# Kernel tuning notes

Hardware: AMD Instinct MI355X
Metric: run time of the kernel (lower is better)

## Reference

```python
import jax, jax.numpy as jnp
import numpy as np

B, T, H, OUT = 65536, 24, 64, 2  # batch, window, num_neurons, 2*predicted_step
P_LAYER, P_TIME = 0.2, 0.2


def _mask(k, p):
    # bernoulli(1-p)/(1-p) variational dropout mask on [B, H]
    return jax.random.bernoulli(k, 1.0 - p, (B, H)).astype(jnp.float32) / (1.0 - p)


def setup_inputs() -> dict:
    key = jax.random.key(0)
    ks = jax.random.split(key, 20)
    u = 1.0 / np.sqrt(H)  # torch LSTMCell default init: U(-1/sqrt(H), 1/sqrt(H))
    xav = np.sqrt(2.0 / (B + H))  # xavier_normal_ std for [B, H] states
    inp = {
        "x": jax.random.normal(ks[0], (B, T, 1), dtype=jnp.float32),
        # LSTMCell 1: input dim 1 -> H; gates stacked [i, f, g, o] like torch
        "W_ih1": jax.random.uniform(ks[1], (4 * H, 1), minval=-u, maxval=u),
        "W_hh1": jax.random.uniform(ks[2], (4 * H, H), minval=-u, maxval=u),
        "b_ih1": jax.random.uniform(ks[3], (4 * H,), minval=-u, maxval=u),
        "b_hh1": jax.random.uniform(ks[4], (4 * H,), minval=-u, maxval=u),
        # LSTMCell 2: H -> H
        "W_ih2": jax.random.uniform(ks[5], (4 * H, H), minval=-u, maxval=u),
        "W_hh2": jax.random.uniform(ks[6], (4 * H, H), minval=-u, maxval=u),
        "b_ih2": jax.random.uniform(ks[7], (4 * H,), minval=-u, maxval=u),
        "b_hh2": jax.random.uniform(ks[8], (4 * H,), minval=-u, maxval=u),
        # output Linear H -> 2, bias hard-set to [0.2, -0.2]
        "W_out": jax.random.uniform(ks[9], (OUT, H), minval=-u, maxval=u),
        "b_out": jnp.array([0.2, -0.2], dtype=jnp.float32),
        # xavier_normal_ initialized states
        "h1_0": jax.random.normal(ks[10], (B, H)) * xav,
        "c1_0": jax.random.normal(ks[11], (B, H)) * xav,
        "h2_0": jax.random.normal(ks[12], (B, H)) * xav,
        "c2_0": jax.random.normal(ks[13], (B, H)) * xav,
        # variational dropout masks, fixed across timesteps
        "m_time1": _mask(ks[14], P_TIME),
        "m_time2": _mask(ks[15], P_TIME),
        "m_layer1": _mask(ks[16], P_LAYER),
        "m_layer2": _mask(ks[17], P_LAYER),
    }
    return inp


def _lstm_cell(x, h, c, W_ih, W_hh, b_ih, b_hh):
    gates = x @ W_ih.T + b_ih + h @ W_hh.T + b_hh  # [B, 4H]
    i, f, g, o = jnp.split(gates, 4, axis=-1)
    c_new = jax.nn.sigmoid(f) * c + jax.nn.sigmoid(i) * jnp.tanh(g)
    h_new = jax.nn.sigmoid(o) * jnp.tanh(c_new)
    return h_new, c_new


def reference(x, W_ih1, W_hh1, b_ih1, b_hh1, W_ih2, W_hh2, b_ih2, b_hh2,
              W_out, b_out, h1_0, c1_0, h2_0, c2_0,
              m_time1, m_time2, m_layer1, m_layer2):
    xs = jnp.transpose(x, (1, 0, 2))  # [T, B, 1]

    def step(carry, x_t):
        h1, c1, h2, c2 = carry
        h1, c1 = _lstm_cell(x_t, h1 * m_time1, c1, W_ih1, W_hh1, b_ih1, b_hh1)
        h1 = h1 * m_layer1
        h2, c2 = _lstm_cell(h1, h2 * m_time2, c2, W_ih2, W_hh2, b_ih2, b_hh2)
        h2 = h2 * m_layer2
        return (h1, c1, h2, c2), None

    (h1, c1, h2, c2), _ = jax.lax.scan(step, (h1_0, c1_0, h2_0, c2_0), xs)
    return h2 @ W_out.T + b_out  # [B, 2]
```

## Files before the change

kernel.cpp:

```cpp
#include <hip/hip_runtime.h>


typedef short short8v __attribute__((ext_vector_type(8)));
typedef float f32x4 __attribute__((ext_vector_type(4)));

#define LOG2E 1.44269504088896340736f

__device__ inline float gsig(float y){
  return __builtin_amdgcn_rcpf(1.0f + __builtin_amdgcn_exp2f(y));
}
__device__ inline float gtanh(float y){
  float s = __builtin_amdgcn_rcpf(1.0f + __builtin_amdgcn_exp2f(y));
  return fmaf(-2.0f, s, 1.0f);
}
__device__ inline float ftanh(float x){
  float e = __builtin_amdgcn_exp2f((2.0f * LOG2E) * x);
  return fmaf(-2.0f, __builtin_amdgcn_rcpf(1.0f + e), 1.0f);
}
__device__ inline unsigned short bf16c(float f){
  unsigned uu = __builtin_bit_cast(unsigned, f);
  uu = (uu + 0x7fffu + ((uu >> 16) & 1u)) >> 16;
  return (unsigned short)uu;
}

#define PK_STORE4(T, I, f0, f1, f2, f3) do{                       \
    unsigned _w01, _w23;                                          \
    asm("v_cvt_pk_bf16_f32 %0, %1, %2" : "=v"(_w01) : "v"(f0), "v"(f1)); \
    asm("v_cvt_pk_bf16_f32 %0, %1, %2" : "=v"(_w23) : "v"(f2), "v"(f3)); \
    (T)[(I)[0]] = (unsigned short)_w01;                           \
    (T)[(I)[1]] = (unsigned short)(_w01 >> 16);                   \
    (T)[(I)[2]] = (unsigned short)_w23;                           \
    (T)[(I)[3]] = (unsigned short)(_w23 >> 16);                   \
  }while(0)

__global__ __launch_bounds__(256, 2) void vlstm_kernel(
    const float* __restrict__ x,
    const float* __restrict__ Wih1, const float* __restrict__ Whh1,
    const float* __restrict__ bih1, const float* __restrict__ bhh1,
    const float* __restrict__ Wih2, const float* __restrict__ Whh2,
    const float* __restrict__ bih2, const float* __restrict__ bhh2,
    const float* __restrict__ Wout, const float* __restrict__ bout,
    const float* __restrict__ h10, const float* __restrict__ c10,
    const float* __restrict__ h20, const float* __restrict__ c20,
    const float* __restrict__ mt1v, const float* __restrict__ mt2v,
    const float* __restrict__ ml1v, const float* __restrict__ ml2v,
    float* __restrict__ out)
{
  __shared__ unsigned short sh1L[2][1024];
  __shared__ unsigned short sh1T[2][1024];
  __shared__ unsigned short sh2T[2][1024];
  __shared__ float h2f[1024];
  __shared__ float xlds[384];

  const int tid = threadIdx.x;
  const int w  = tid >> 6;
  const int l  = tid & 63;
  const int hi = l >> 4;
  const int lo = l & 15;
  const int u  = 16 * w + lo;

  float b1v[4], b2v[4], wiv[4];
  short8v fr1[4][2], frI[4][2], frH[4][2];
#pragma unroll
  for (int j = 0; j < 4; ++j){
    const float sc = (j == 2) ? (2.0f * LOG2E) : (-LOG2E);
    int n = u + 64 * j;
    b1v[j] = sc * (bih1[n] + bhh1[n]);
    b2v[j] = sc * (bih2[n] + bhh2[n]);
    wiv[j] = sc * Wih1[n];
#pragma unroll
    for (int kk = 0; kk < 2; ++kk){
      int off = n * 64 + 32 * kk + 8 * hi;
      short8v s;
#pragma unroll
      for (int e = 0; e < 8; ++e) s[e] = (short)bf16c(sc * Whh1[off + e]);
      fr1[j][kk] = s;
#pragma unroll
      for (int e = 0; e < 8; ++e) s[e] = (short)bf16c(sc * Wih2[off + e]);
      frI[j][kk] = s;
#pragma unroll
      for (int e = 0; e < 8; ++e) s[e] = (short)bf16c(sc * Whh2[off + e]);
      frH[j][kk] = s;
    }
  }

  int wIdx[4];
#pragma unroll
  for (int r = 0; r < 4; ++r){
    int m = 4 * hi + r;
    wIdx[r] = ((m * 128 + u * 2) ^ ((m & 7) << 4)) >> 1;
  }
  int rIdx[2];
#pragma unroll
  for (int kk = 0; kk < 2; ++kk){
    rIdx[kk] = ((lo * 128 + kk * 64 + hi * 16) ^ ((lo & 7) << 4)) >> 1;
  }

  const int row0 = blockIdx.x * 16;

  for (int idx = tid; idx < 384; idx += 256){
    int r = idx / 24, tt = idx - r * 24;
    xlds[tt * 16 + r] = x[(row0 + r) * 24 + tt];
  }
  float c1r[4], c2r[4], ml1r[4], ml2r[4], mt1r[4], mt2r[4];
  float h1i[4], h2i[4];
#pragma unroll
  for (int r = 0; r < 4; ++r){
    int gofs = (row0 + 4 * hi + r) * 64 + u;
    c1r[r]  = c10[gofs];  c2r[r]  = c20[gofs];
    ml1r[r] = ml1v[gofs]; ml2r[r] = ml2v[gofs];
    mt1r[r] = mt1v[gofs]; mt2r[r] = mt2v[gofs];
    h1i[r] = h10[gofs] * mt1r[r];
    h2i[r] = h20[gofs] * mt2r[r];
  }
  PK_STORE4(sh1T[0], wIdx, h1i[0], h1i[1], h1i[2], h1i[3]);
  PK_STORE4(sh2T[0], wIdx, h2i[0], h2i[1], h2i[2], h2i[3]);
  __syncthreads();

  short8v a1[2], at2[2];
  a1[0] = *(const short8v*)&sh1T[0][rIdx[0]];
  a1[1] = *(const short8v*)&sh1T[0][rIdx[1]];

  int P = 0;
#pragma unroll 1
  for (int t = 0; t < 24; ++t){
    const int Q = P ^ 1;
    f32x4 xv = *(const f32x4*)&xlds[t * 16 + 4 * hi];

    f32x4 gt[4];
#pragma unroll
    for (int j = 0; j < 4; ++j){
      f32x4 acc;
#pragma unroll
      for (int r = 0; r < 4; ++r) acc[r] = fmaf(xv[r], wiv[j], b1v[j]);
      acc = __builtin_amdgcn_mfma_f32_16x16x32_bf16(a1[0], fr1[j][0], acc, 0, 0, 0);
      acc = __builtin_amdgcn_mfma_f32_16x16x32_bf16(a1[1], fr1[j][1], acc, 0, 0, 0);
      gt[j] = acc;
    }
    float h1l[4], h1t[4];
#pragma unroll
    for (int r = 0; r < 4; ++r){
      float ti = gsig(gt[0][r]);
      float tf = gsig(gt[1][r]);
      float tg = gtanh(gt[2][r]);
      float to = gsig(gt[3][r]);
      float cn = fmaf(tf, c1r[r], ti * tg);
      c1r[r] = cn;
      h1l[r] = to * ftanh(cn) * ml1r[r];
      h1t[r] = h1l[r] * mt1r[r];
    }
    PK_STORE4(sh1L[Q], wIdx, h1l[0], h1l[1], h1l[2], h1l[3]);
    PK_STORE4(sh1T[Q], wIdx, h1t[0], h1t[1], h1t[2], h1t[3]);

    __syncthreads();

    short8v a2[2];
    a2[0]  = *(const short8v*)&sh1L[Q][rIdx[0]];
    a2[1]  = *(const short8v*)&sh1L[Q][rIdx[1]];
    a1[0]  = *(const short8v*)&sh1T[Q][rIdx[0]];
    a1[1]  = *(const short8v*)&sh1T[Q][rIdx[1]];
    at2[0] = *(const short8v*)&sh2T[P][rIdx[0]];
    at2[1] = *(const short8v*)&sh2T[P][rIdx[1]];

#pragma unroll
    for (int j = 0; j < 4; ++j){
      f32x4 acc;
#pragma unroll
      for (int r = 0; r < 4; ++r) acc[r] = b2v[j];
      acc = __builtin_amdgcn_mfma_f32_16x16x32_bf16(a2[0],  frI[j][0], acc, 0, 0, 0);
      acc = __builtin_amdgcn_mfma_f32_16x16x32_bf16(a2[1],  frI[j][1], acc, 0, 0, 0);
      acc = __builtin_amdgcn_mfma_f32_16x16x32_bf16(at2[0], frH[j][0], acc, 0, 0, 0);
      acc = __builtin_amdgcn_mfma_f32_16x16x32_bf16(at2[1], frH[j][1], acc, 0, 0, 0);
      gt[j] = acc;
    }
    float h2t[4];
#pragma unroll
    for (int r = 0; r < 4; ++r){
      float ti = gsig(gt[0][r]);
      float tf = gsig(gt[1][r]);
      float tg = gtanh(gt[2][r]);
      float to = gsig(gt[3][r]);
      float cn = fmaf(tf, c2r[r], ti * tg);
      c2r[r] = cn;
      float h2l = to * ftanh(cn) * ml2r[r];
      h2t[r] = h2l * mt2r[r];
      if (t == 23) h2f[(4 * hi + r) * 64 + u] = h2l;
    }
    PK_STORE4(sh2T[Q], wIdx, h2t[0], h2t[1], h2t[2], h2t[3]);

    P = Q;
  }
  __syncthreads();

  if (tid < 32){
    int r = tid & 15, o = tid >> 4;
    float acc = bout[o];
#pragma unroll 8
    for (int uu = 0; uu < 64; ++uu)
      acc = fmaf(h2f[r * 64 + uu], Wout[o * 64 + uu], acc);
    out[(row0 + r) * 2 + o] = acc;
  }
}

extern "C" void kernel_launch(void* const* d_in, const int* in_sizes, int n_in,
                              void* d_out, int out_size, void* d_ws, size_t ws_size,
                              hipStream_t stream)
{
  vlstm_kernel<<<dim3(4096), dim3(256), 0, stream>>>(
      (const float*)d_in[0],  (const float*)d_in[1],  (const float*)d_in[2],
      (const float*)d_in[3],  (const float*)d_in[4],  (const float*)d_in[5],
      (const float*)d_in[6],  (const float*)d_in[7],  (const float*)d_in[8],
      (const float*)d_in[9],  (const float*)d_in[10], (const float*)d_in[11],
      (const float*)d_in[12], (const float*)d_in[13], (const float*)d_in[14],
      (const float*)d_in[15], (const float*)d_in[16], (const float*)d_in[17],
      (const float*)d_in[18], (float*)d_out);
}
```

Before: 351.4 us.

## Raise occupancy to three blocks per CU via AGPR weights and packed masks

Raises the launch-bounds minimum from two to three blocks per CU. To fit the register budget it forces most bf16 weight fragments into AGPRs through an empty asm constraint and packs the four dropout masks into bf16 pairs, unpacked on each use. The aim is more resident waves to hide MFMA and transcendental latency in the serial recurrence. Each step now pays extra unpack ALU work, AGPR-to-VGPR moves may appear, and bf16 masks stay exact only because the mask values (0 and 1.25) are representable.

```diff
diff --git a/kernel.cpp b/kernel.cpp
--- a/kernel.cpp
+++ b/kernel.cpp
@@ -21,6 +21,10 @@
   unsigned uu = __builtin_bit_cast(unsigned, f);
   uu = (uu + 0x7fffu + ((uu >> 16) & 1u)) >> 16;
   return (unsigned short)uu;
+}
+__device__ inline float unpk(unsigned p, int h){
+  unsigned b = h ? (p & 0xffff0000u) : (p << 16);
+  return __builtin_bit_cast(float, b);
 }
 
 #define PK_STORE4(T, I, f0, f1, f2, f3) do{                       \
@@ -33,7 +37,7 @@
     (T)[(I)[3]] = (unsigned short)(_w23 >> 16);                   \
   }while(0)
 
-__global__ __launch_bounds__(256, 2) void vlstm_kernel(
+__global__ __launch_bounds__(256, 3) void vlstm_kernel(
     const float* __restrict__ x,
     const float* __restrict__ Wih1, const float* __restrict__ Whh1,
     const float* __restrict__ bih1, const float* __restrict__ bhh1,
@@ -84,6 +88,14 @@
     }
   }
 
+  asm volatile("" :
+    "+a"(fr1[0][0]), "+a"(fr1[0][1]), "+a"(fr1[1][0]), "+a"(fr1[1][1]),
+    "+a"(fr1[2][0]), "+a"(fr1[2][1]), "+a"(fr1[3][0]), "+a"(fr1[3][1]),
+    "+a"(frI[0][0]), "+a"(frI[0][1]), "+a"(frI[1][0]), "+a"(frI[1][1]),
+    "+a"(frI[2][0]), "+a"(frI[2][1]), "+a"(frI[3][0]), "+a"(frI[3][1]),
+    "+a"(frH[0][0]), "+a"(frH[0][1]), "+a"(frH[1][0]), "+a"(frH[1][1]),
+    "+a"(frH[2][0]));
+
   int wIdx[4];
 #pragma unroll
   for (int r = 0; r < 4; ++r){
@@ -102,19 +114,29 @@
     int r = idx / 24, tt = idx - r * 24;
     xlds[tt * 16 + r] = x[(row0 + r) * 24 + tt];
   }
-  float c1r[4], c2r[4], ml1r[4], ml2r[4], mt1r[4], mt2r[4];
-  float h1i[4], h2i[4];
-#pragma unroll
-  for (int r = 0; r < 4; ++r){
-    int gofs = (row0 + 4 * hi + r) * 64 + u;
-    c1r[r]  = c10[gofs];  c2r[r]  = c20[gofs];
-    ml1r[r] = ml1v[gofs]; ml2r[r] = ml2v[gofs];
-    mt1r[r] = mt1v[gofs]; mt2r[r] = mt2v[gofs];
-    h1i[r] = h10[gofs] * mt1r[r];
-    h2i[r] = h20[gofs] * mt2r[r];
-  }
-  PK_STORE4(sh1T[0], wIdx, h1i[0], h1i[1], h1i[2], h1i[3]);
-  PK_STORE4(sh2T[0], wIdx, h2i[0], h2i[1], h2i[2], h2i[3]);
+  float c1r[4], c2r[4];
+  unsigned ml1p[2], mt1p[2], ml2p[2], mt2p[2];
+  {
+    float mlt1[4], mtt1[4], mlt2[4], mtt2[4], h1i[4], h2i[4];
+#pragma unroll
+    for (int r = 0; r < 4; ++r){
+      int gofs = (row0 + 4 * hi + r) * 64 + u;
+      c1r[r]  = c10[gofs];  c2r[r]  = c20[gofs];
+      mlt1[r] = ml1v[gofs]; mlt2[r] = ml2v[gofs];
+      mtt1[r] = mt1v[gofs]; mtt2[r] = mt2v[gofs];
+      h1i[r] = h10[gofs] * mtt1[r];
+      h2i[r] = h20[gofs] * mtt2[r];
+    }
+#pragma unroll
+    for (int pr = 0; pr < 2; ++pr){
+      ml1p[pr] = (unsigned)bf16c(mlt1[2*pr]) | ((unsigned)bf16c(mlt1[2*pr+1]) << 16);
+      mt1p[pr] = (unsigned)bf16c(mtt1[2*pr]) | ((unsigned)bf16c(mtt1[2*pr+1]) << 16);
+      ml2p[pr] = (unsigned)bf16c(mlt2[2*pr]) | ((unsigned)bf16c(mlt2[2*pr+1]) << 16);
+      mt2p[pr] = (unsigned)bf16c(mtt2[2*pr]) | ((unsigned)bf16c(mtt2[2*pr+1]) << 16);
+    }
+    PK_STORE4(sh1T[0], wIdx, h1i[0], h1i[1], h1i[2], h1i[3]);
+    PK_STORE4(sh2T[0], wIdx, h2i[0], h2i[1], h2i[2], h2i[3]);
+  }
   __syncthreads();
 
   short8v a1[2], at2[2];
@@ -146,8 +168,8 @@
       float to = gsig(gt[3][r]);
       float cn = fmaf(tf, c1r[r], ti * tg);
       c1r[r] = cn;
-      h1l[r] = to * ftanh(cn) * ml1r[r];
-      h1t[r] = h1l[r] * mt1r[r];
+      h1l[r] = to * ftanh(cn) * unpk(ml1p[r >> 1], r & 1);
+      h1t[r] = h1l[r] * unpk(mt1p[r >> 1], r & 1);
     }
     PK_STORE4(sh1L[Q], wIdx, h1l[0], h1l[1], h1l[2], h1l[3]);
     PK_STORE4(sh1T[Q], wIdx, h1t[0], h1t[1], h1t[2], h1t[3]);
@@ -182,8 +204,8 @@
       float to = gsig(gt[3][r]);
       float cn = fmaf(tf, c2r[r], ti * tg);
       c2r[r] = cn;
-      float h2l = to * ftanh(cn) * ml2r[r];
-      h2t[r] = h2l * mt2r[r];
+      float h2l = to * ftanh(cn) * unpk(ml2p[r >> 1], r & 1);
+      h2t[r] = h2l * unpk(mt2p[r >> 1], r & 1);
       if (t == 23) h2f[(4 * hi + r) * 64 + u] = h2l;
     }
     PK_STORE4(sh2T[Q], wIdx, h2t[0], h2t[1], h2t[2], h2t[3]);
```

Result: slower. 873.5 us (+148.6%).
